# Optimization experiments

Hardware: AMD Instinct MI355X
Metric: run time of the kernel (lower is better)

The kernel has to match this reference:

```python
import jax, jax.numpy as jnp
import numpy as np

SIGMA = 1.0
SQRT2 = float(np.sqrt(2.0))


def setup_inputs() -> dict:
    key = jax.random.key(0)
    k1, k2 = jax.random.split(key)
    B, L = 128, 1024
    preds = jax.random.normal(k1, (B, L), dtype=jnp.float32)
    # integer relevance grades 0..4, stored as float as in the torch module
    target = jax.random.randint(k2, (B, L), 0, 5).astype(jnp.float32)
    return {"preds": preds, "target": target}


def reference(preds, target):
    B, L = preds.shape
    # pairwise diff [B, L, L]: diff[b,i,j] = preds[b,i] - preds[b,j]
    diff = preds[:, :, None] - preds[:, None, :]
    # Normal(0, sigma*sqrt(2)).cdf(diff) == ndtr(diff / (sigma*sqrt(2)))
    p = jax.scipy.special.ndtr(diff / (SIGMA * SQRT2))
    # zero the diagonal (i == j) before summing
    eye = jnp.eye(L, dtype=bool)
    p = jnp.where(eye[None, :, :], 0.0, p)
    expected_ranks = 1.0 + p.sum(axis=2)  # [B, L]

    gains = 2.0 ** target - 1.0
    discounts = jnp.log2(expected_ranks + 1.0)
    dcg = (gains / discounts).sum(axis=1)  # [B]

    ideal_target = jnp.sort(target, axis=1)[:, ::-1]  # descending
    ideal_gains = 2.0 ** ideal_target - 1.0
    ideal_discounts = jnp.log2(jnp.arange(1, L + 1, dtype=jnp.float32) + 1.0)
    idcg = (ideal_gains / ideal_discounts).sum(axis=1)  # [B]

    ndcg = dcg / (idcg + 1e-10)
    return -ndcg.mean()
```

## Files before the change

kernel.cpp:

```cpp
#include <hip/hip_runtime.h>
#include <hip/hip_fp16.h>

#define B 128
#define L 1024
#define NTILE 24
#define TSTRIDE 576

#if __has_builtin(__builtin_amdgcn_exp2f)
#define EXP2(x) __builtin_amdgcn_exp2f(x)
#else
#define EXP2(x) __expf((x) * 0.6931471805599453f)
#endif

typedef unsigned int uint4v __attribute__((ext_vector_type(4)));

#define WS2     (B * NTILE * TSTRIDE)
#define WS_ACC  (WS2 + B * L)
#define WS_GCTR (WS_ACC + 1)

#define K1f -1.6279072f
#define K2f -0.9299637f
#define K3f -0.1074808f

__device__ __forceinline__ __half2 term2v(unsigned int du, __half2 pi2,
                                          __half2 k1, __half2 k2, __half2 k3,
                                          __half2 one2) {
    __half2 pj = __builtin_bit_cast(__half2, du);
    __half2 d  = __hsub2(pi2, pj);
    unsigned int dbits = __builtin_bit_cast(unsigned int, d);
    __half2 a  = __builtin_bit_cast(__half2, dbits & 0x7fff7fffu);
    __half2 t  = __hfma2(k3, a, k2);
    __half2 u  = __hfma2(t,  a, k1);
    __half2 w  = __hmul2(a, u);
    __half2 e  = __halves2half2(hexp2(__low2half(w)),
                                hexp2(__high2half(w)));
    __half2 r  = __hsub2(one2, e);
    unsigned int rs = (dbits & 0x80008000u)
                    | (__builtin_bit_cast(unsigned int, r) & 0x7fff7fffu);
    return __builtin_bit_cast(__half2, rs);
}

__global__ __launch_bounds__(256, 8) void pair_kernel(const float* __restrict__ preds,
                                                      const float* __restrict__ target,
                                                      float* __restrict__ ws) {
    __shared__ __align__(16) unsigned char smem[2048 + 8192 + 8192];
    __half* sph = (__half*)smem;
    float* rowLDS = (float*)(smem + 2048);
    unsigned int* colLDS = (unsigned int*)(smem + 2048 + 8192);
    float* col2LDS = (float*)(smem + 2048 + 8192);

    const int blk = blockIdx.x;
    const int b   = blk >> 4;
    const int kk  = blk & 15;
    const int tid = threadIdx.x;
    const int il  = tid & 63;
    const int jq  = tid >> 6;

    if (blk == 0 && tid == 0) {
        ws[WS_ACC] = 0.0f;
        ((int*)ws)[WS_GCTR] = 0;
    }

    const float* prow = preds + b * L;
    float4 v4 = reinterpret_cast<const float4*>(prow)[tid];
    reinterpret_cast<__half2*>(sph)[tid * 2 + 0] = __floats2half2_rn(0.5f * v4.x, 0.5f * v4.y);
    reinterpret_cast<__half2*>(sph)[tid * 2 + 1] = __floats2half2_rn(0.5f * v4.z, 0.5f * v4.w);
    __syncthreads();

    const __half2 k1   = __floats2half2_rn(K1f, K1f);
    const __half2 k2   = __floats2half2_rn(K2f, K2f);
    const __half2 k3   = __floats2half2_rn(K3f, K3f);
    const __half2 one2 = __floats2half2_rn(1.0f, 1.0f);
    const __half2 z2   = __floats2half2_rn(0.0f, 0.0f);

    const int ntl = (kk < 8) ? 2 : 1;
    for (int tt = 0; tt < ntl; ++tt) {
        const int tl = tt ? (23 - kk) : kk;
        const int r  = (tl >= 16) ? 1 : 0;
        const int q  = r ? (tl - 8) : tl;

        const uint4v* cp4 = reinterpret_cast<const uint4v*>(sph + q * 64 + jq * 16);
        uint4v pq0 = cp4[0], pq1 = cp4[1];
        unsigned int pjb[8] = {pq0.x, pq0.y, pq0.z, pq0.w, pq1.x, pq1.y, pq1.z, pq1.w};

        __half2 colacc[8] = {z2, z2, z2, z2, z2, z2, z2, z2};

        const int r8 = r << 3;
        for (int rr = 0; rr < 8; ++rr) {
            const int s = r8 + rr;
            if (s > q) break;
            const bool ca = (s < q);
            const __half2 pi2 = __half2half2(sph[(s << 6) + il]);
            __half2 A = z2, Bc = z2;
            #pragma unroll
            for (int m = 0; m < 8; ++m) {
                __half2 tm = term2v(pjb[m], pi2, k1, k2, k3, one2);
                if (m < 4) A = __hadd2(A, tm); else Bc = __hadd2(Bc, tm);
                if (ca) colacc[m] = __hadd2(colacc[m], tm);
            }
            float2 fA = __half22float2(A), fB = __half22float2(Bc);
            rowLDS[(rr << 8) + (jq << 6) + il] = (fA.x + fA.y) + (fB.x + fB.y);
        }

        #pragma unroll
        for (int m = 0; m < 8; ++m)
            colLDS[((jq << 3) + m) * 64 + il] = __builtin_bit_cast(unsigned int, colacc[m]);
        __syncthreads();

        float* wst = ws + (b * NTILE + tl) * TSTRIDE;

        #pragma unroll
        for (int h = 0; h < 2; ++h) {
            int rho = tid + (h << 8);
            int rrx = rho >> 6, ilx = rho & 63;
            float v = (rowLDS[(rrx << 8) + ilx]       + rowLDS[(rrx << 8) + 64 + ilx])
                    + (rowLDS[(rrx << 8) + 128 + ilx] + rowLDS[(rrx << 8) + 192 + ilx]);
            wst[rho] = v;
        }

        float sx = 0.0f, sy = 0.0f;
        {
            int cp = tid & 31, ilq = tid >> 5;
            const uint4v* cl = reinterpret_cast<const uint4v*>(colLDS + cp * 64 + ilq * 8);
            uint4v c0 = cl[0], c1 = cl[1];
            unsigned int cc[8] = {c0.x, c0.y, c0.z, c0.w, c1.x, c1.y, c1.z, c1.w};
            #pragma unroll
            for (int m = 0; m < 8; ++m) {
                float2 f = __half22float2(__builtin_bit_cast(__half2, cc[m]));
                sx += f.x; sy += f.y;
            }
        }
        __syncthreads();
        {
            int cp = tid & 31, ilq = tid >> 5;
            col2LDS[ilq * 64 + cp * 2 + 0] = sx;
            col2LDS[ilq * 64 + cp * 2 + 1] = sy;
        }
        __syncthreads();

        if (tid < 64) {
            float cs = 0.0f;
            #pragma unroll
            for (int g = 0; g < 8; ++g) cs += col2LDS[g * 64 + tid];
            wst[512 + tid] = cs;
        }
        __syncthreads();
    }
}

__global__ __launch_bounds__(256) void gather_kernel(const float* __restrict__ target,
                                                     float* __restrict__ ws) {
    const int blk = blockIdx.x;
    const int b   = blk >> 2;
    const int i   = ((blk & 3) << 8) + threadIdx.x;
    const int u   = i >> 6;
    const int rb  = u >> 3;
    const int rho = i & 511;
    const int i6  = i & 63;
    const int b24 = b * NTILE;

    float rowsum = 0.0f;
    for (int qq = u; qq < 16; ++qq)
        rowsum += ws[(b24 + qq + (rb << 3)) * TSTRIDE + rho];
    float cols = 0.0f;
    if (u >= 1) cols += ws[(b24 + u) * TSTRIDE + 512 + i6];
    if (u >= 9) cols += ws[(b24 + u + 8) * TSTRIDE + 512 + i6];

    float Es  = rowsum - cols;
    float er1 = 513.5f + 0.5f * Es;
    float g   = EXP2(target[b * L + i]) - 1.0f;
    ws[WS2 + b * L + i] = g * __builtin_amdgcn_rcpf(__log2f(er1));
}

__global__ __launch_bounds__(256) void finish_kernel(const float* __restrict__ target,
                                                     float* __restrict__ ws,
                                                     float* __restrict__ out) {
    __shared__ unsigned long long cred[256];
    __shared__ float2 fred[256];

    const int b   = blockIdx.x;
    const int tid = threadIdx.x;
    const float* trow = target + b * L;

    unsigned long long cnt = 0ull;
    #pragma unroll
    for (int k = 0; k < 4; ++k) {
        float t = trow[tid + k * 256];
        cnt += ((unsigned long long)(t > 3.5f) << 48)
             + ((unsigned long long)(t > 2.5f) << 32)
             + ((unsigned long long)(t > 1.5f) << 16)
             + ((unsigned long long)(t > 0.5f));
    }
    cred[tid] = cnt;
    __syncthreads();
    #pragma unroll
    for (int s = 128; s > 0; s >>= 1) {
        if (tid < (unsigned)s) cred[tid] += cred[tid + s];
        __syncthreads();
    }
    unsigned long long tot = cred[0];
    const int n4 = (int)(tot >> 48) & 0xFFFF;
    const int n3 = (int)(tot >> 32) & 0xFFFF;
    const int n2 = (int)(tot >> 16) & 0xFFFF;
    const int n1 = (int)(tot)       & 0xFFFF;

    float idcg_p = 0.0f;
    float dcg_p  = 0.0f;
    #pragma unroll
    for (int k = 0; k < 4; ++k) {
        int pos = tid + 1 + k * 256;
        float gain = (pos <= n4) ? 15.0f : (pos <= n3) ? 7.0f :
                     (pos <= n2) ? 3.0f  : (pos <= n1) ? 1.0f : 0.0f;
        idcg_p += gain * __builtin_amdgcn_rcpf(__log2f((float)pos + 1.0f));
        dcg_p  += ws[WS2 + b * L + tid + k * 256];
    }

    fred[tid] = make_float2(idcg_p, dcg_p);
    __syncthreads();
    #pragma unroll
    for (int s = 128; s > 0; s >>= 1) {
        if (tid < (unsigned)s) {
            float2 x = fred[tid], y = fred[tid + s];
            fred[tid] = make_float2(x.x + y.x, x.y + y.y);
        }
        __syncthreads();
    }

    if (tid == 0) {
        float ndcg = fred[0].y / (fred[0].x + 1e-10f);
        atomicAdd(&ws[WS_ACC], ndcg);
        __threadfence();
        int old = atomicAdd((int*)ws + WS_GCTR, 1);
        if (old == B - 1) {
            float acc = atomicAdd(&ws[WS_ACC], 0.0f);
            out[0] = -acc * (1.0f / (float)B);
        }
    }
}

extern "C" void kernel_launch(void* const* d_in, const int* in_sizes, int n_in,
                              void* d_out, int out_size, void* d_ws, size_t ws_size,
                              hipStream_t stream) {
    const float* preds  = (const float*)d_in[0];
    const float* target = (const float*)d_in[1];
    float* out = (float*)d_out;
    float* ws  = (float*)d_ws;

    pair_kernel<<<B * 16, 256, 0, stream>>>(preds, target, ws);
    gather_kernel<<<B * 4, 256, 0, stream>>>(target, ws);
    finish_kernel<<<B, 256, 0, stream>>>(target, ws, out);
}
```

Measured before the change: 89.00 us.

## Fuse gather and finish kernels using per-row atomic last-block reduction

Merges the gather and finish kernels into one launch. Each block reduces its own DCG contributions and grade counts in shared memory, then adds them into per-row atomics. The last of the four blocks for a row computes IDCG and the NDCG term. This removes one kernel launch and the round trip of the per-element DCG array through global memory. It also unrolls the row-sum loop with predication instead of a variable trip count. The cost is extra atomics, a threadfence-based last-block handshake, and more workspace words that must be zeroed in the first kernel.

```diff
diff --git a/kernel.cpp b/kernel.cpp
--- a/kernel.cpp
+++ b/kernel.cpp
@@ -14,9 +14,13 @@
 
 typedef unsigned int uint4v __attribute__((ext_vector_type(4)));
 
-#define WS2     (B * NTILE * TSTRIDE)
-#define WS_ACC  (WS2 + B * L)
-#define WS_GCTR (WS_ACC + 1)
+#define WS_TAIL (B * NTILE * TSTRIDE)
+#define WS_DCG  (WS_TAIL)
+#define WS_QCTR (WS_TAIL + 128)
+#define WS_CNT  (WS_TAIL + 256)
+#define WS_ACC  (WS_TAIL + 512)
+#define WS_GCTR (WS_TAIL + 513)
+#define WS_ZWORDS 514
 
 #define K1f -1.6279072f
 #define K2f -0.9299637f
@@ -56,9 +60,9 @@
     const int il  = tid & 63;
     const int jq  = tid >> 6;
 
-    if (blk == 0 && tid == 0) {
-        ws[WS_ACC] = 0.0f;
-        ((int*)ws)[WS_GCTR] = 0;
+    if (blk == 0) {
+        for (int k = tid; k < WS_ZWORDS; k += 256)
+            ((unsigned int*)ws)[WS_TAIL + k] = 0u;
     }
 
     const float* prow = preds + b * L;
@@ -148,11 +152,17 @@
     }
 }
 
-__global__ __launch_bounds__(256) void gather_kernel(const float* __restrict__ target,
-                                                     float* __restrict__ ws) {
+__global__ __launch_bounds__(256) void gf_kernel(const float* __restrict__ target,
+                                                 float* __restrict__ ws,
+                                                 float* __restrict__ out) {
+    __shared__ unsigned long long cred[256];
+    __shared__ float fred[256];
+    __shared__ int lastflag;
+
     const int blk = blockIdx.x;
     const int b   = blk >> 2;
-    const int i   = ((blk & 3) << 8) + threadIdx.x;
+    const int tid = threadIdx.x;
+    const int i   = ((blk & 3) << 8) + tid;
     const int u   = i >> 6;
     const int rb  = u >> 3;
     const int rho = i & 511;
@@ -160,81 +170,80 @@
     const int b24 = b * NTILE;
 
     float rowsum = 0.0f;
-    for (int qq = u; qq < 16; ++qq)
-        rowsum += ws[(b24 + qq + (rb << 3)) * TSTRIDE + rho];
-    float cols = 0.0f;
-    if (u >= 1) cols += ws[(b24 + u) * TSTRIDE + 512 + i6];
-    if (u >= 9) cols += ws[(b24 + u + 8) * TSTRIDE + 512 + i6];
+    #pragma unroll
+    for (int qq = 0; qq < 16; ++qq) {
+        float v = ws[(b24 + qq + (rb << 3)) * TSTRIDE + rho];
+        rowsum += (qq >= u) ? v : 0.0f;
+    }
+    float c1v = ws[(b24 + u) * TSTRIDE + 512 + i6];
+    float c2v = ws[(b24 + u + 8) * TSTRIDE + 512 + i6];
+    float cols = ((u >= 1) ? c1v : 0.0f) + ((u >= 9) ? c2v : 0.0f);
 
     float Es  = rowsum - cols;
     float er1 = 513.5f + 0.5f * Es;
-    float g   = EXP2(target[b * L + i]) - 1.0f;
-    ws[WS2 + b * L + i] = g * __builtin_amdgcn_rcpf(__log2f(er1));
-}
-
-__global__ __launch_bounds__(256) void finish_kernel(const float* __restrict__ target,
-                                                     float* __restrict__ ws,
-                                                     float* __restrict__ out) {
-    __shared__ unsigned long long cred[256];
-    __shared__ float2 fred[256];
-
-    const int b   = blockIdx.x;
-    const int tid = threadIdx.x;
-    const float* trow = target + b * L;
-
-    unsigned long long cnt = 0ull;
-    #pragma unroll
-    for (int k = 0; k < 4; ++k) {
-        float t = trow[tid + k * 256];
-        cnt += ((unsigned long long)(t > 3.5f) << 48)
-             + ((unsigned long long)(t > 2.5f) << 32)
-             + ((unsigned long long)(t > 1.5f) << 16)
-             + ((unsigned long long)(t > 0.5f));
-    }
+    float tgt = target[b * L + i];
+    float g   = EXP2(tgt) - 1.0f;
+    float contrib = g * __builtin_amdgcn_rcpf(__log2f(er1));
+
+    unsigned long long cnt =
+          ((unsigned long long)(tgt > 3.5f) << 48)
+        + ((unsigned long long)(tgt > 2.5f) << 32)
+        + ((unsigned long long)(tgt > 1.5f) << 16)
+        + ((unsigned long long)(tgt > 0.5f));
+
     cred[tid] = cnt;
+    fred[tid] = contrib;
     __syncthreads();
     #pragma unroll
     for (int s = 128; s > 0; s >>= 1) {
-        if (tid < (unsigned)s) cred[tid] += cred[tid + s];
-        __syncthreads();
-    }
-    unsigned long long tot = cred[0];
+        if (tid < (unsigned)s) {
+            cred[tid] += cred[tid + s];
+            fred[tid] += fred[tid + s];
+        }
+        __syncthreads();
+    }
+
+    unsigned long long* cntA = (unsigned long long*)(ws + WS_CNT);
+    if (tid == 0) {
+        atomicAdd(&ws[WS_DCG + b], fred[0]);
+        atomicAdd(&cntA[b], cred[0]);
+        __threadfence();
+        int pos = atomicAdd((int*)ws + WS_QCTR + b, 1);
+        lastflag = (pos == 3);
+    }
+    __syncthreads();
+    if (!lastflag) return;
+
+    unsigned long long tot = atomicAdd(&cntA[b], 0ull);
     const int n4 = (int)(tot >> 48) & 0xFFFF;
     const int n3 = (int)(tot >> 32) & 0xFFFF;
     const int n2 = (int)(tot >> 16) & 0xFFFF;
     const int n1 = (int)(tot)       & 0xFFFF;
 
     float idcg_p = 0.0f;
-    float dcg_p  = 0.0f;
     #pragma unroll
     for (int k = 0; k < 4; ++k) {
         int pos = tid + 1 + k * 256;
         float gain = (pos <= n4) ? 15.0f : (pos <= n3) ? 7.0f :
                      (pos <= n2) ? 3.0f  : (pos <= n1) ? 1.0f : 0.0f;
         idcg_p += gain * __builtin_amdgcn_rcpf(__log2f((float)pos + 1.0f));
-        dcg_p  += ws[WS2 + b * L + tid + k * 256];
-    }
-
-    fred[tid] = make_float2(idcg_p, dcg_p);
+    }
+    fred[tid] = idcg_p;
     __syncthreads();
     #pragma unroll
     for (int s = 128; s > 0; s >>= 1) {
-        if (tid < (unsigned)s) {
-            float2 x = fred[tid], y = fred[tid + s];
-            fred[tid] = make_float2(x.x + y.x, x.y + y.y);
-        }
+        if (tid < (unsigned)s) fred[tid] += fred[tid + s];
         __syncthreads();
     }
 
     if (tid == 0) {
-        float ndcg = fred[0].y / (fred[0].x + 1e-10f);
+        float dcg  = atomicAdd(&ws[WS_DCG + b], 0.0f);
+        float ndcg = dcg / (fred[0] + 1e-10f);
         atomicAdd(&ws[WS_ACC], ndcg);
         __threadfence();
         int old = atomicAdd((int*)ws + WS_GCTR, 1);
-        if (old == B - 1) {
-            float acc = atomicAdd(&ws[WS_ACC], 0.0f);
-            out[0] = -acc * (1.0f / (float)B);
-        }
+        if (old == B - 1)
+            out[0] = -atomicAdd(&ws[WS_ACC], 0.0f) * (1.0f / (float)B);
     }
 }
 
@@ -247,6 +256,5 @@
     float* ws  = (float*)d_ws;
 
     pair_kernel<<<B * 16, 256, 0, stream>>>(preds, target, ws);
-    gather_kernel<<<B * 4, 256, 0, stream>>>(target, ws);
-    finish_kernel<<<B, 256, 0, stream>>>(target, ws, out);
-}
+    gf_kernel<<<B * 4, 256, 0, stream>>>(target, ws, out);
+}
```

Result: slower. 91.29 us (+2.6%).
